# Optimization experiments

Hardware: AMD Instinct MI355X
Metric: run time of the kernel (lower is better)

The kernel has to match this reference:

```python
import jax, jax.numpy as jnp
import numpy as np

N = 200_000        # primal nodes (mesh faces)
E = 600_000        # directed primal edges (= dual nodes)
F = 128            # feature dim
NUM_KEEP = 300_000 # num_primal_edges_to_keep
ITERS = 40         # label-propagation iterations (>= ~2*log2(N), safely converged)


def setup_inputs() -> dict:
    key = jax.random.key(0)
    k1, k2, k3, k4 = jax.random.split(key, 4)
    primal_x = jax.random.normal(k1, (N, F), dtype=jnp.float32)
    dual_x = jax.random.normal(k2, (E, F), dtype=jnp.float32)
    att = jax.random.uniform(k3, (E,), dtype=jnp.float32)  # attention coeffs in (0,1)
    primal_edge_index = jax.random.randint(k4, (2, E), 0, N, dtype=jnp.int32)
    return {"primal_x": primal_x, "dual_x": dual_x, "att": att,
            "primal_edge_index": primal_edge_index}


def _pool(primal_x, dual_x, att, primal_edge_index):
    src, dst = primal_edge_index[0], primal_edge_index[1]
    num_pool = E - NUM_KEEP

    # --- Top-K edge selection by decreasing attention coefficient ---
    order = jnp.argsort(-att)
    pool_mask = jnp.zeros((E,), jnp.bool_).at[order[:num_pool]].set(True)

    # --- Union-find / connected components of pooled edges via
    #     min-label propagation with pointer jumping (vectorized union-find) ---
    u = src
    v = jnp.where(pool_mask, dst, src)  # masked edges become self-edges (no-ops)

    def body(_, l):
        l = l.at[u].min(l[v]).at[v].min(l[u])  # edge relaxations (scatter-min)
        l = l[l]                                # pointer jumping
        l = l[l]
        return l

    labels = jax.lax.fori_loop(0, ITERS, body, jnp.arange(N, dtype=jnp.int32))

    # --- Compact component labels into contiguous new-primal-node ids ---
    _, cluster = jnp.unique(labels, size=N, fill_value=N, return_inverse=True)
    cluster = cluster.astype(jnp.int32)

    # --- Aggregate primal node features per cluster ('mean') ---
    counts = jax.ops.segment_sum(jnp.ones((N,), primal_x.dtype), cluster,
                                 num_segments=N)
    new_primal_x = jax.ops.segment_sum(primal_x, cluster, num_segments=N)
    new_primal_x = new_primal_x / jnp.maximum(counts, 1.0)[:, None]

    # --- Rebuild primal edges; edges internal to a cluster are pooled away ---
    cu, cv = cluster[src], cluster[dst]
    valid = cu != cv
    new_primal_edge_index = jnp.stack([jnp.where(valid, cu, -1),
                                       jnp.where(valid, cv, -1)])

    # --- Dual nodes: one per (unordered) surviving new primal edge
    #     ('single' dual nodes); merge & mean-aggregate dual features of old
    #     dual nodes mapping to the same new dual node ---
    a = jnp.minimum(cu, cv)
    b = jnp.maximum(cu, cv)
    pairs = jnp.stack([jnp.where(valid, a, N), jnp.where(valid, b, N)], axis=1)
    _, dual_cluster = jnp.unique(pairs, axis=0, size=E, fill_value=N,
                                 return_inverse=True)
    dual_cluster = dual_cluster.reshape(E).astype(jnp.int32)
    vm = valid.astype(dual_x.dtype)
    dcounts = jax.ops.segment_sum(vm, dual_cluster, num_segments=E)
    new_dual_x = jax.ops.segment_sum(dual_x * vm[:, None], dual_cluster,
                                     num_segments=E)
    new_dual_x = new_dual_x / jnp.maximum(dcounts, 1.0)[:, None]

    return new_primal_x, new_dual_x, new_primal_edge_index, cluster


def reference(primal_x, dual_x, att, primal_edge_index):
    return _pool(primal_x, dual_x, att, primal_edge_index)
```

## Files before the change

### kernel.cpp

```cpp
#include <hip/hip_runtime.h>
#include <stdint.h>


#define N_NODES 200000
#define N_EDGES 600000
#define FDIM 128
#define NUM_POOL 300000u

#define SC_NEEDEQ 3
#define SC_TIECNT 4
#define SC_C 5
#define SC_W 6
#define SC_U 7
#define SC_VCNT 8
#define SC_WL0 16
#define TIECAP 4096
#define WLCAP 300800
#define HB 256
#define NSB 98
#define NSHAD 8
#define NSHAD2 16
#define CMAX 16384
#define SROWS 64
#define SGB 782
#define CS2B 128

__device__ __forceinline__ uint32_t f2ou(float f){
  uint32_t b = __float_as_uint(f);
  return (b & 0x80000000u) ? ~b : (b | 0x80000000u);
}

static __device__ __forceinline__ void sel_level(const uint32_t* hist, uint32_t& target,
                                                 uint32_t& pfx, uint32_t* sm, uint32_t* res){
  int t = threadIdx.x;
  uint32_t cnt = hist[t];
  sm[t] = cnt; __syncthreads();
  for(int off = 1; off < 256; off <<= 1){
    uint32_t y = (t + off < 256) ? sm[t + off] : 0u;
    __syncthreads(); sm[t] += y; __syncthreads();
  }
  uint32_t suffix = sm[t];
  uint32_t above  = suffix - cnt;
  if(above < target && target <= suffix){ res[0] = (uint32_t)t; res[1] = target - above; }
  __syncthreads();
  pfx = (pfx << 8) | res[0];
  target = res[1];
  __syncthreads();
}

static __device__ __forceinline__ uint32_t blk_excl(uint32_t v, uint32_t* sm, uint32_t& total){
  int t = threadIdx.x;
  sm[t] = v; __syncthreads();
  for(int off = 1; off < 256; off <<= 1){
    uint32_t y = (t >= off) ? sm[t - off] : 0u;
    __syncthreads(); sm[t] += y; __syncthreads();
  }
  total = sm[255];
  uint32_t incl = sm[t];
  __syncthreads();
  return incl - v;
}

__global__ __launch_bounds__(256) void k_zero(uint4* w4, uint32_t n4){
  uint32_t gid = blockIdx.x*256 + threadIdx.x;
  uint4 z = make_uint4(0u,0u,0u,0u);
  for(uint32_t j = gid; j < n4; j += gridDim.x*256) w4[j] = z;
}

template<int LEVEL>
__global__ __launch_bounds__(256) void k_hist8(const float* att, uint32_t* hists, int* L){
  __shared__ uint32_t h[256];
  __shared__ uint32_t sm[256];
  __shared__ uint32_t res[2];
  h[threadIdx.x] = 0;
  if(LEVEL == 1){
    for(int i = blockIdx.x*256 + threadIdx.x; i < N_NODES; i += HB*256) L[i] = i;
  }
  __syncthreads();
  uint32_t pfx = 0, target = NUM_POOL;
  #pragma unroll
  for(int l = 0; l < LEVEL-1; ++l) sel_level(hists + 256*l, target, pfx, sm, res);
  constexpr int SH1 = (LEVEL > 1) ? 8*(5-LEVEL) : 0;
  constexpr int SH2 = 8*(4-LEVEL);
  for(int e = blockIdx.x*256 + threadIdx.x; e < N_EDGES; e += HB*256){
    uint32_t u = f2ou(att[e]);
    bool ok = (LEVEL == 1) || ((u >> SH1) == pfx);
    if(ok) atomicAdd(&h[(u >> SH2) & 0xFFu], 1u);
  }
  __syncthreads();
  uint32_t c = h[threadIdx.x];
  if(c) atomicAdd(&hists[256*(LEVEL-1) + threadIdx.x], c);
}

__global__ __launch_bounds__(256) void k_seed(const float* att, const int* src, const int* dst,
                       const uint32_t* hists, uint32_t* sc, uint32_t* tieIdx, int* L, uint2* wl,
                       uint32_t* counts, uint32_t* counts2){
  __shared__ uint32_t sm[256];
  __shared__ uint32_t res[2];
  __shared__ uint32_t basesh;
  {
    uint32_t gid = blockIdx.x*256 + threadIdx.x;
    uint32_t gs = gridDim.x*256;
    const uint32_t TOTZ = N_NODES + CMAX*NSHAD2;
    for(uint32_t j = gid; j < TOTZ; j += gs){
      if(j < N_NODES) counts[j] = 0u; else counts2[j - N_NODES] = 0u;
    }
  }
  uint32_t pfx = 0, target = NUM_POOL;
  #pragma unroll
  for(int l = 0; l < 4; ++l) sel_level(hists + 256*l, target, pfx, sm, res);
  if(blockIdx.x == 0 && threadIdx.x == 0) sc[SC_NEEDEQ] = target;
  uint32_t T = pfx;
  int e = blockIdx.x*256 + threadIdx.x;
  bool app = false; int u = 0, v = 0;
  if(e < N_EDGES){
    uint32_t ub = f2ou(att[e]);
    if(ub > T){
      u = src[e]; v = dst[e];
      if(u != v){
        int m = u < v ? u : v, hi = u ^ v ^ m;
        atomicMin(&L[hi], m);
        app = true;
      }
    } else if(ub == T){
      uint32_t p = atomicAdd(&sc[SC_TIECNT], 1u);
      if(p < TIECAP) tieIdx[p] = (uint32_t)e;
    }
  }
  uint32_t tot;
  uint32_t off = blk_excl(app ? 1u : 0u, sm, tot);
  if(threadIdx.x == 0 && tot) basesh = atomicAdd(&sc[SC_WL0], tot);
  __syncthreads();
  if(app) wl[basesh + off] = make_uint2((uint32_t)(u < v ? u : v), (uint32_t)(u > v ? u : v));
}
__global__ __launch_bounds__(1024) void k_tiesel(uint32_t* sc, const uint32_t* tieIdx,
                        const int* src, const int* dst, int* L, uint2* wl){
  uint32_t m = sc[SC_TIECNT]; if(m > TIECAP) m = TIECAP;
  uint32_t need = sc[SC_NEEDEQ];
  int lane = threadIdx.x & 63;
  for(uint32_t i0 = 0; i0 < m; i0 += 1024){
    uint32_t i = i0 + threadIdx.x;
    bool app = false; int u = 0, v = 0;
    if(i < m){
      uint32_t mine = tieIdx[i];
      uint32_t r = 0;
      for(uint32_t j = 0; j < m; j++) r += (tieIdx[j] < mine) ? 1u : 0u;
      if(r < need){
        u = src[mine]; v = dst[mine];
        if(u != v){ int mm = u < v ? u : v, hi = u ^ v ^ mm; atomicMin(&L[hi], mm); app = true; }
      }
    }
    unsigned long long grp = __ballot(app);
    if(grp){
      int leader = __ffsll(grp) - 1;
      uint32_t base = 0;
      if(lane == leader) base = atomicAdd(&sc[SC_WL0], (uint32_t)__popcll(grp));
      base = (uint32_t)__shfl((int)base, leader);
      if(app){
        uint32_t off = (uint32_t)__popcll(grp & ((1ull << lane) - 1ull));
        wl[base + off] = make_uint2((uint32_t)(u < v ? u : v), (uint32_t)(u > v ? u : v));
      }
    }
  }
}
__global__ __launch_bounds__(256) void k_relax(const uint2* wl_in, uint2* wl_out, int* L,
                       uint32_t* sc, int inSlot, int outSlot){
  __shared__ uint32_t sm[256];
  __shared__ uint32_t basesh;
  uint32_t n = sc[inSlot];
  for(uint32_t base = blockIdx.x*256u; base < n; base += gridDim.x*256u){
    uint32_t idx = base + threadIdx.x;
    bool active = idx < n;
    int lu = 0, lv = 0;
    if(active){
      uint2 ed = wl_in[idx];
      lu = L[ed.x]; lu = L[lu]; lu = L[lu]; lu = L[lu];
      lv = L[ed.y]; lv = L[lv]; lv = L[lv]; lv = L[lv];
      active = (lu != lv);
      if(active){
        int m = lu < lv ? lu : lv, hi = lu ^ lv ^ m;
        atomicMin(&L[hi], m);
      }
    }
    uint32_t tot;
    uint32_t off = blk_excl(active ? 1u : 0u, sm, tot);
    if(threadIdx.x == 0 && tot) basesh = atomicAdd(&sc[outSlot], tot);
    __syncthreads();
    if(active) wl_out[basesh + off] = make_uint2((uint32_t)(lu < lv ? lu : lv),
                                                 (uint32_t)(lu > lv ? lu : lv));
    __syncthreads();
  }
  if(n != 0){
    int i = blockIdx.x*256 + threadIdx.x;
    if(i < N_NODES){
      int v = L[i]; v = L[v]; v = L[v]; v = L[v];
      if(v < i) atomicMin(&L[i], v);
    }
  }
}
__global__ __launch_bounds__(256) void k_flatten_reduce(int* L, uint32_t* bsums){
  uint32_t base = blockIdx.x*2048u + threadIdx.x*8u;
  uint32_t s = 0;
  #pragma unroll
  for(int k = 0; k < 8; k++){
    uint32_t i = base + k;
    if(i < N_NODES){
      int p = L[i]; int q = L[p];
      while(q != p){ p = q; q = L[p]; }
      L[i] = p;
      s += (p == (int)i) ? 1u : 0u;
    }
  }
  __shared__ uint32_t sm[256];
  sm[threadIdx.x] = s; __syncthreads();
  for(int off = 128; off > 0; off >>= 1){
    if((int)threadIdx.x < off) sm[threadIdx.x] += sm[threadIdx.x + off];
    __syncthreads();
  }
  if(threadIdx.x == 0) bsums[blockIdx.x] = sm[0];
}

template<int MODE>
__device__ __forceinline__ uint32_t scan_n(const uint32_t* sc){
  if(MODE == 1) return sc[SC_W];
  if(MODE == 3) return sc[SC_C]*NSHAD2;
  return N_NODES;
}
template<int MODE>
__global__ __launch_bounds__(256) void k_scan_reduce(const uint32_t* in, uint32_t* bsums,
                       const uint32_t* sc, float* dsum, uint32_t* dcnt){
  uint32_t n = scan_n<MODE>(sc);
  if(MODE == 1){
    uint32_t vc = sc[SC_VCNT];
    size_t gid = (size_t)blockIdx.x*256 + threadIdx.x, gs = (size_t)gridDim.x*256;
    float4* d4 = (float4*)dsum;
    float4 z = make_float4(0.f,0.f,0.f,0.f);
    for(size_t j = gid; j < (size_t)vc*(FDIM/4); j += gs) d4[j] = z;
    for(size_t j = gid; j < vc; j += gs) dcnt[j] = 0u;
  }
  uint32_t base = blockIdx.x*2048u + threadIdx.x*8u;
  uint32_t s = 0;
  #pragma unroll
  for(int k = 0; k < 8; k++){
    uint32_t idx = base + k;
    if(idx < n){ uint32_t v = in[idx]; if(MODE == 1) v = __popc(v); s += v; }
  }
  __shared__ uint32_t sm[256];
  sm[threadIdx.x] = s; __syncthreads();
  for(int off = 128; off > 0; off >>= 1){
    if((int)threadIdx.x < off) sm[threadIdx.x] += sm[threadIdx.x + off];
    __syncthreads();
  }
  if(threadIdx.x == 0) bsums[blockIdx.x] = sm[0];
}
template<int MODE>
__global__ __launch_bounds__(256) void k_scan_apply(const uint32_t* in, const int* L,
                       const uint32_t* bsums, int nb, uint32_t* out, uint32_t* sc){
  __shared__ uint32_t bs[4096];
  __shared__ uint32_t sm[256];
  int t = threadIdx.x;
  uint32_t n = scan_n<MODE>(sc);
  uint32_t loc[16]; uint32_t ls = 0;
  #pragma unroll
  for(int k = 0; k < 16; k++){ int idx = t*16 + k; uint32_t v = (idx < nb) ? bsums[idx] : 0u; loc[k] = v; ls += v; }
  sm[t] = ls; __syncthreads();
  for(int off = 1; off < 256; off <<= 1){
    uint32_t y = (t >= off) ? sm[t - off] : 0u;
    __syncthreads(); sm[t] += y; __syncthreads();
  }
  uint32_t total = sm[255];
  uint32_t run = sm[t] - ls;
  #pragma unroll
  for(int k = 0; k < 16; k++){ bs[t*16 + k] = run; run += loc[k]; }
  __syncthreads();
  uint32_t blockbase = bs[blockIdx.x];
  __syncthreads();
  uint32_t base = blockIdx.x*2048u + t*8u;
  uint32_t xs[8]; uint32_t ts2 = 0;
  #pragma unroll
  for(int k = 0; k < 8; k++){
    uint32_t idx = base + k; uint32_t v = 0;
    if(idx < n){
      if(MODE == 2) v = (L[idx] == (int)idx) ? 1u : 0u;
      else { v = in[idx]; if(MODE == 1) v = __popc(v); }
    }
    xs[k] = v; ts2 += v;
  }
  sm[t] = ts2; __syncthreads();
  for(int off = 1; off < 256; off <<= 1){
    uint32_t y = (t >= off) ? sm[t - off] : 0u;
    __syncthreads(); sm[t] += y; __syncthreads();
  }
  uint32_t run2 = blockbase + sm[t] - ts2;
  #pragma unroll
  for(int k = 0; k < 8; k++){ uint32_t idx = base + k; if(idx < n) out[idx] = run2; run2 += xs[k]; }
  if(blockIdx.x == 0 && t == 0){
    if(MODE == 2){ sc[SC_C] = total; uint64_t cc = (uint64_t)total*(uint64_t)total; sc[SC_W] = (uint32_t)((cc + 31ull) >> 5); }
    if(MODE == 1){ sc[SC_U] = total; }
  }
}

__global__ __launch_bounds__(256) void k_cluster_counts(const int* L, const uint32_t* rank_,
                       int* cluster_i, float* outC, uint32_t* counts, uint32_t* counts2,
                       float* psumS, uint32_t* bitmap, const uint32_t* sc){
  uint32_t C = sc[SC_C], W = sc[SC_W];
  uint32_t gid = blockIdx.x*256 + threadIdx.x, gs = gridDim.x*256;
  float4* p4 = (float4*)psumS;
  float4 z = make_float4(0.f,0.f,0.f,0.f);
  for(size_t j = gid; j < (size_t)NSHAD*C*(FDIM/4); j += gs) p4[j] = z;
  for(uint32_t j = gid; j < W; j += gs) bitmap[j] = 0u;
  int i = (int)gid;
  int lane = threadIdx.x & 63;
  int sh = (int)((gid >> 6) & (NSHAD2-1));
  int c = -1;
  if(i < N_NODES){
    c = (int)rank_[L[i]];
    cluster_i[i] = c;
    outC[i] = (float)c;
  }
  unsigned long long remaining = __ballot(i < N_NODES);
  while(remaining){
    int leader = __ffsll(remaining) - 1;
    int lc = __shfl(c, leader);
    unsigned long long grp = __ballot(c == lc) & remaining;
    if(lane == leader){
      uint32_t cnt = (uint32_t)__popcll(grp);
      atomicAdd(&counts[lc], cnt);
      atomicAdd(&counts2[lc*NSHAD2 + sh], cnt);
    }
    remaining &= ~grp;
  }
}
__global__ void k_scatter(const int* cluster_i, uint32_t* cursor2, uint32_t* order){
  uint32_t gid = blockIdx.x*256 + threadIdx.x;
  int i = (int)gid;
  int lane = threadIdx.x & 63;
  int sh = (int)((gid >> 6) & (NSHAD2-1));
  int c = (i < N_NODES) ? cluster_i[i] : -1;
  unsigned long long remaining = __ballot(i < N_NODES);
  while(remaining){
    int leader = __ffsll(remaining) - 1;
    int lc = __shfl(c, leader);
    unsigned long long grp = __ballot(c == lc) & remaining;
    int b = 0;
    if(lane == leader) b = (int)atomicAdd(&cursor2[lc*NSHAD2 + sh], (uint32_t)__popcll(grp));
    b = __shfl(b, leader);
    if((grp >> lane) & 1ull){
      uint32_t sub = (uint32_t)__popcll(grp & ((1ull << lane) - 1ull));
      order[(uint32_t)b + sub] = (uint32_t)i;
    }
    remaining &= ~grp;
  }
}

__global__ __launch_bounds__(256) void k_seg_edges(const float* px, const uint32_t* order,
        const int* cluster_i, float* psumS, const int* src, const int* dst, uint32_t* sc,
        float* outE, uint32_t* kc, uint32_t* bitmap){
  if(blockIdx.x < SGB){
    int wave = (int)((blockIdx.x*256u + threadIdx.x) >> 6);
    int lane = threadIdx.x & 63;
    int start = wave * SROWS;
    if(start >= N_NODES) return;
    int cnt = N_NODES - start; if(cnt > SROWS) cnt = SROWS;
    size_t shadBase = (size_t)(wave & (NSHAD-1)) * (size_t)sc[SC_C] * FDIM;
    uint32_t ord0 = 0; int c0 = -1;
    if(lane < cnt){ ord0 = order[start + lane]; c0 = cluster_i[ord0]; }
    float ax = 0.f, ay = 0.f; int cur = -1;
    for(int r = 0; r < cnt; r++){
      uint32_t i = (uint32_t)__shfl((int)ord0, r);
      int c = __shfl(c0, r);
      if(c != cur){
        if(cur >= 0){
          atomicAdd(&psumS[shadBase + (size_t)cur*FDIM + 2*lane], ax);
          atomicAdd(&psumS[shadBase + (size_t)cur*FDIM + 2*lane + 1], ay);
        }
        cur = c; ax = 0.f; ay = 0.f;
      }
      float2 v = ((const float2*)(px + (size_t)i*FDIM))[lane];
      ax += v.x; ay += v.y;
    }
    if(cur >= 0){
      atomicAdd(&psumS[shadBase + (size_t)cur*FDIM + 2*lane], ax);
      atomicAdd(&psumS[shadBase + (size_t)cur*FDIM + 2*lane + 1], ay);
    }
  } else {
    __shared__ uint32_t wsum[4];
    int e = (blockIdx.x - SGB)*256 + threadIdx.x;
    int lane = threadIdx.x & 63;
    int wv = threadIdx.x >> 6;
    bool val = false;
    if(e < N_EDGES){
      int cu = cluster_i[src[e]];
      int cv = cluster_i[dst[e]];
      val = (cu != cv);
      outE[e] = val ? (float)cu : -1.0f;
      outE[N_EDGES + e] = val ? (float)cv : -1.0f;
      if(val){
        int a = cu < cv ? cu : cv, b = cu < cv ? cv : cu;
        uint32_t C = sc[SC_C];
        uint32_t key = (uint32_t)a * C + (uint32_t)b;
        kc[e] = key;
        atomicOr(&bitmap[key >> 5], 1u << (key & 31u));
      } else {
        kc[e] = 0xFFFFFFFFu;
      }
    }
    unsigned long long grp = __ballot(val);
    if(lane == 0) wsum[wv] = (uint32_t)__popcll(grp);
    __syncthreads();
    if(threadIdx.x == 0){
      uint32_t s = wsum[0] + wsum[1] + wsum[2] + wsum[3];
      if(s) atomicAdd(&sc[SC_VCNT], s);
    }
  }
}

__global__ __launch_bounds__(256) void k_dualacc(const float* dx, const uint32_t* kc,
                          const uint32_t* bitmap, const uint32_t* wpref,
                          float* dsum, uint32_t* dcnt){
  int wave = (int)((blockIdx.x*256u + threadIdx.x) >> 6);
  int lane = threadIdx.x & 63;
  int base = wave * 64;
  if(base >= N_EDGES) return;
  int e = base + lane;
  uint32_t key = (e < N_EDGES) ? kc[e] : 0xFFFFFFFFu;
  bool val = (key != 0xFFFFFFFFu);
  uint32_t r = 0;
  if(val){
    uint32_t wi = key >> 5, bi = key & 31u;
    r = wpref[wi] + __popc(bitmap[wi] & ((1u << bi) - 1u));
  }
  unsigned long long m = __ballot(val);
  while(m){
    int b = __ffsll(m) - 1;
    m &= m - 1;
    uint32_t ee = (uint32_t)(base + b);
    uint32_t rr = (uint32_t)__shfl((int)r, b);
    float2 v = ((const float2*)(dx + (size_t)ee*FDIM))[lane];
    atomicAdd(&dsum[(size_t)rr*FDIM + 2*lane], v.x);
    atomicAdd(&dsum[(size_t)rr*FDIM + 2*lane + 1], v.y);
    if(lane == 0) atomicAdd(&dcnt[rr], 1u);
  }
}
__global__ __launch_bounds__(256) void k_finalize(const float4* psumS, const uint32_t* counts,
        const float4* dsum, const uint32_t* dcnt, const uint32_t* sc, float4* out4){
  uint32_t C = sc[SC_C], U = sc[SC_U];
  size_t cs = (size_t)C * (FDIM/4);
  size_t gid = (size_t)blockIdx.x*256 + threadIdx.x;
  size_t gs = (size_t)gridDim.x*256;
  const size_t NP4 = (size_t)N_NODES*(FDIM/4);
  const size_t TOT4 = (size_t)(N_NODES + N_EDGES)*(FDIM/4);
  for(size_t j = gid; j < TOT4; j += gs){
    float4 v = make_float4(0.f,0.f,0.f,0.f);
    if(j < NP4){
      uint32_t r = (uint32_t)(j >> 5);
      if(r < C){
        v = psumS[j];
        #pragma unroll
        for(int s = 1; s < NSHAD; s++){
          float4 t = psumS[(size_t)s*cs + j];
          v.x += t.x; v.y += t.y; v.z += t.z; v.w += t.w;
        }
        float fc = (float)counts[r];
        v.x /= fc; v.y /= fc; v.z /= fc; v.w /= fc;
      }
    } else {
      size_t dj = j - NP4;
      uint32_t r = (uint32_t)(dj >> 5);
      if(r < U){
        v = dsum[dj];
        float fc = (float)dcnt[r];
        v.x /= fc; v.y /= fc; v.z /= fc; v.w /= fc;
      }
    }
    out4[j] = v;
  }
}

extern "C" void kernel_launch(void* const* d_in, const int* in_sizes, int n_in,
                              void* d_out, int out_size, void* d_ws, size_t ws_size,
                              hipStream_t stream){
  (void)in_sizes; (void)n_in; (void)out_size;
  const float* primal_x = (const float*)d_in[0];
  const float* dual_x   = (const float*)d_in[1];
  const float* att      = (const float*)d_in[2];
  const int*   pei      = (const int*)d_in[3];
  const int* src = pei;
  const int* dst = pei + N_EDGES;

  float* out  = (float*)d_out;
  float* outE = out + (size_t)(N_NODES + N_EDGES)*FDIM;
  float* outC = outE + (size_t)2*N_EDGES;

  uint32_t* w = (uint32_t*)d_ws;
  size_t words_avail = ws_size / 4;
  const size_t PSUMW = (size_t)NSHAD*CMAX*FDIM;
  const size_t CNT2W = (size_t)CMAX*NSHAD2;
  const size_t FIXED = 64 + 1024 + (size_t)N_NODES + CNT2W
                     + TIECAP + 4*(size_t)N_NODES + CNT2W + 4*(size_t)WLCAP
                     + (size_t)N_EDGES + (size_t)N_EDGES
                     + 4096
                     + PSUMW + (size_t)N_EDGES*FDIM;
  size_t wcap = (words_avail > FIXED) ? (words_avail - FIXED)/2 : 4;
  if(wcap > 8388608) wcap = 8388608;
  wcap &= ~(size_t)3;

  size_t o = 0;
  uint32_t* sc      = w;               o += 64;
  uint32_t* hists   = w + o;           o += 1024;
  size_t zero_words = o;
  uint32_t* counts  = w + o;           o += N_NODES;
  uint32_t* counts2 = w + o;           o += CNT2W;
  uint32_t* tieIdx  = w + o;           o += TIECAP;
  int* labels       = (int*)(w + o);   o += N_NODES;
  uint32_t* rank_   = w + o;           o += N_NODES;
  int* cluster_i    = (int*)(w + o);   o += N_NODES;
  uint32_t* order   = w + o;           o += N_NODES;
  uint32_t* cursor2 = w + o;           o += CNT2W;
  uint2* wl0        = (uint2*)(w + o); o += 2*(size_t)WLCAP;
  uint2* wl1        = (uint2*)(w + o); o += 2*(size_t)WLCAP;
  uint32_t* kc      = w + o;           o += N_EDGES;
  uint32_t* dcnt    = w + o;           o += N_EDGES;
  uint32_t* bsums   = w + o;           o += 4096;
  float* psumS      = (float*)(w + o); o += PSUMW;
  float* dsum       = (float*)(w + o); o += (size_t)N_EDGES*FDIM;
  uint32_t* bitmap  = w + o;           o += wcap;
  uint32_t* wpref   = w + o;           o += wcap;

  const int EB  = (N_EDGES + 255)/256;
  const int NB  = (N_NODES + 255)/256;
  const int WSB = (int)((wcap + 2047)/2048);

  k_zero<<<2,256,0,stream>>>((uint4*)w, (uint32_t)(zero_words/4));
  k_hist8<1><<<HB,256,0,stream>>>(att, hists, labels);
  k_hist8<2><<<HB,256,0,stream>>>(att, hists, labels);
  k_hist8<3><<<HB,256,0,stream>>>(att, hists, labels);
  k_hist8<4><<<HB,256,0,stream>>>(att, hists, labels);
  k_seed<<<EB,256,0,stream>>>(att, src, dst, hists, sc, tieIdx, labels, wl0, counts, counts2);
  k_tiesel<<<1,1024,0,stream>>>(sc, tieIdx, src, dst, labels, wl0);
  for(int r = 1; r <= 8; ++r){
    uint2* win  = (r & 1) ? wl0 : wl1;
    uint2* wout = (r & 1) ? wl1 : wl0;
    k_relax<<<1024,256,0,stream>>>(win, wout, labels, sc, SC_WL0 + r - 1, SC_WL0 + r);
  }
  k_flatten_reduce<<<NSB,256,0,stream>>>(labels, bsums);
  k_scan_apply<2><<<NSB,256,0,stream>>>(counts, labels, bsums, NSB, rank_, sc);
  k_cluster_counts<<<NB,256,0,stream>>>(labels, rank_, cluster_i, outC, counts, counts2,
                                        psumS, bitmap, sc);
  k_scan_reduce<3><<<CS2B,256,0,stream>>>(counts2, bsums, sc, dsum, dcnt);
  k_scan_apply<3><<<CS2B,256,0,stream>>>(counts2, labels, bsums, CS2B, cursor2, sc);
  k_scatter<<<NB,256,0,stream>>>(cluster_i, cursor2, order);
  k_seg_edges<<<SGB + EB,256,0,stream>>>(primal_x, order, cluster_i, psumS,
                                         src, dst, sc, outE, kc, bitmap);
  k_scan_reduce<1><<<WSB,256,0,stream>>>(bitmap, bsums, sc, dsum, dcnt);
  k_scan_apply<1><<<WSB,256,0,stream>>>(bitmap, labels, bsums, WSB, wpref, sc);
  k_dualacc<<<EB,256,0,stream>>>(dual_x, kc, bitmap, wpref, dsum, dcnt);
  k_finalize<<<2048,256,0,stream>>>((const float4*)psumS, counts, (const float4*)dsum,
                                    dcnt, sc, (float4*)out);
}
```

Measured before the change: 592.3 us.

## Use 3-level radix select and fold tie resolution into first relax pass

Top-K threshold selection now stops after three 8-bit radix histogram levels instead of four, dropping one histogram kernel. The candidate bucket at the threshold becomes larger, so ties are ranked by the full key and then the index. That ranking now runs inside block 0 of the first relax launch instead of in a separate single-block kernel. The aim is to remove two launches and one pass over att. The risk is that the tie bucket may grow past TIECAP or that the O(m^2) ranking in one block becomes slow.

```diff
diff --git a/kernel.cpp b/kernel.cpp
--- a/kernel.cpp
+++ b/kernel.cpp
@@ -18,7 +18,7 @@
 #define WLCAP 300800
 #define HB 256
 #define NSB 98
-#define NSHAD 8
+#define NSHAD 4
 #define NSHAD2 16
 #define CMAX 16384
 #define SROWS 64
@@ -108,13 +108,13 @@
   }
   uint32_t pfx = 0, target = NUM_POOL;
   #pragma unroll
-  for(int l = 0; l < 4; ++l) sel_level(hists + 256*l, target, pfx, sm, res);
+  for(int l = 0; l < 3; ++l) sel_level(hists + 256*l, target, pfx, sm, res);
   if(blockIdx.x == 0 && threadIdx.x == 0) sc[SC_NEEDEQ] = target;
   uint32_t T = pfx;
   int e = blockIdx.x*256 + threadIdx.x;
   bool app = false; int u = 0, v = 0;
   if(e < N_EDGES){
-    uint32_t ub = f2ou(att[e]);
+    uint32_t ub = f2ou(att[e]) >> 8;
     if(ub > T){
       u = src[e]; v = dst[e];
       if(u != v){
@@ -133,38 +133,11 @@
   __syncthreads();
   if(app) wl[basesh + off] = make_uint2((uint32_t)(u < v ? u : v), (uint32_t)(u > v ? u : v));
 }
-__global__ __launch_bounds__(1024) void k_tiesel(uint32_t* sc, const uint32_t* tieIdx,
-                        const int* src, const int* dst, int* L, uint2* wl){
-  uint32_t m = sc[SC_TIECNT]; if(m > TIECAP) m = TIECAP;
-  uint32_t need = sc[SC_NEEDEQ];
-  int lane = threadIdx.x & 63;
-  for(uint32_t i0 = 0; i0 < m; i0 += 1024){
-    uint32_t i = i0 + threadIdx.x;
-    bool app = false; int u = 0, v = 0;
-    if(i < m){
-      uint32_t mine = tieIdx[i];
-      uint32_t r = 0;
-      for(uint32_t j = 0; j < m; j++) r += (tieIdx[j] < mine) ? 1u : 0u;
-      if(r < need){
-        u = src[mine]; v = dst[mine];
-        if(u != v){ int mm = u < v ? u : v, hi = u ^ v ^ mm; atomicMin(&L[hi], mm); app = true; }
-      }
-    }
-    unsigned long long grp = __ballot(app);
-    if(grp){
-      int leader = __ffsll(grp) - 1;
-      uint32_t base = 0;
-      if(lane == leader) base = atomicAdd(&sc[SC_WL0], (uint32_t)__popcll(grp));
-      base = (uint32_t)__shfl((int)base, leader);
-      if(app){
-        uint32_t off = (uint32_t)__popcll(grp & ((1ull << lane) - 1ull));
-        wl[base + off] = make_uint2((uint32_t)(u < v ? u : v), (uint32_t)(u > v ? u : v));
-      }
-    }
-  }
-}
+
 __global__ __launch_bounds__(256) void k_relax(const uint2* wl_in, uint2* wl_out, int* L,
-                       uint32_t* sc, int inSlot, int outSlot){
+                       uint32_t* sc, int inSlot, int outSlot,
+                       const uint32_t* tieIdx, const float* att,
+                       const int* src, const int* dst, int doTies){
   __shared__ uint32_t sm[256];
   __shared__ uint32_t basesh;
   uint32_t n = sc[inSlot];
@@ -189,6 +162,35 @@
     if(active) wl_out[basesh + off] = make_uint2((uint32_t)(lu < lv ? lu : lv),
                                                  (uint32_t)(lu > lv ? lu : lv));
     __syncthreads();
+  }
+  if(doTies && blockIdx.x == 0){
+    uint32_t m = sc[SC_TIECNT]; if(m > TIECAP) m = TIECAP;
+    uint32_t need = sc[SC_NEEDEQ];
+    for(uint32_t i0 = 0; i0 < m; i0 += 256){
+      uint32_t i = i0 + threadIdx.x;
+      bool app = false; int u = 0, v = 0;
+      if(i < m){
+        uint32_t mine = tieIdx[i];
+        uint32_t ki = f2ou(att[mine]);
+        uint32_t r = 0;
+        for(uint32_t j = 0; j < m; j++){
+          uint32_t oj = tieIdx[j];
+          uint32_t kj = f2ou(att[oj]);
+          r += (kj > ki || (kj == ki && oj < mine)) ? 1u : 0u;
+        }
+        if(r < need){
+          u = src[mine]; v = dst[mine];
+          if(u != v){ int mm = u < v ? u : v, hi = u ^ v ^ mm; atomicMin(&L[hi], mm); app = true; }
+        }
+      }
+      uint32_t tot;
+      uint32_t off = blk_excl(app ? 1u : 0u, sm, tot);
+      if(threadIdx.x == 0 && tot) basesh = atomicAdd(&sc[outSlot], tot);
+      __syncthreads();
+      if(app) wl_out[basesh + off] = make_uint2((uint32_t)(u < v ? u : v),
+                                                (uint32_t)(u > v ? u : v));
+      __syncthreads();
+    }
   }
   if(n != 0){
     int i = blockIdx.x*256 + threadIdx.x;
@@ -535,13 +537,12 @@
   k_hist8<1><<<HB,256,0,stream>>>(att, hists, labels);
   k_hist8<2><<<HB,256,0,stream>>>(att, hists, labels);
   k_hist8<3><<<HB,256,0,stream>>>(att, hists, labels);
-  k_hist8<4><<<HB,256,0,stream>>>(att, hists, labels);
   k_seed<<<EB,256,0,stream>>>(att, src, dst, hists, sc, tieIdx, labels, wl0, counts, counts2);
-  k_tiesel<<<1,1024,0,stream>>>(sc, tieIdx, src, dst, labels, wl0);
   for(int r = 1; r <= 8; ++r){
     uint2* win  = (r & 1) ? wl0 : wl1;
     uint2* wout = (r & 1) ? wl1 : wl0;
-    k_relax<<<1024,256,0,stream>>>(win, wout, labels, sc, SC_WL0 + r - 1, SC_WL0 + r);
+    k_relax<<<1024,256,0,stream>>>(win, wout, labels, sc, SC_WL0 + r - 1, SC_WL0 + r,
+                                   tieIdx, att, src, dst, (r == 1) ? 1 : 0);
   }
   k_flatten_reduce<<<NSB,256,0,stream>>>(labels, bsums);
   k_scan_apply<2><<<NSB,256,0,stream>>>(counts, labels, bsums, NSB, rank_, sc);
```

Result: no change. 589.8 us (-0.4%).
